# Kernel tuning notes

Measured on AMD Instinct MI355X. Metric: run time of the kernel, lower is better.

Reference implementation:

```python
import jax, jax.numpy as jnp
import numpy as np

D_MODEL = 256
D_INNER = 512   # expand=2 * d_model
D_STATE = 16
D_CONV = 4
DT_RANK = 16    # ceil(d_model/16)
N_BLOCKS = 5
BATCH = 8192
INPUT_DIM = 2048
NUM_CLASSES = 8


def setup_inputs() -> dict:
    key = jax.random.key(0)
    ks = jax.random.split(key, 10)
    rn = lambda k, shape, s: jax.random.normal(k, shape, jnp.float32) * s
    inp = {}
    inp['x'] = rn(ks[0], (BATCH, INPUT_DIM), 1.0)
    # preprocess Linear(input_dim, 256)
    inp['W_pre'] = rn(ks[1], (D_MODEL, INPUT_DIM), 0.02)
    inp['b_pre'] = jnp.zeros((D_MODEL,), jnp.float32)
    # per-block Mamba params, stacked over N_BLOCKS
    inp['in_proj_w'] = rn(ks[2], (N_BLOCKS, 2 * D_INNER, D_MODEL), 0.02)
    inp['conv_w'] = rn(ks[3], (N_BLOCKS, D_INNER, 1, D_CONV), 0.1)   # depthwise, groups=d_inner
    inp['conv_b'] = jnp.zeros((N_BLOCKS, D_INNER), jnp.float32)
    inp['x_proj_w'] = rn(ks[4], (N_BLOCKS, DT_RANK + 2 * D_STATE, D_INNER), 0.02)
    inp['dt_proj_w'] = rn(ks[5], (N_BLOCKS, D_INNER, DT_RANK), 0.1)
    inp['dt_proj_b'] = rn(ks[6], (N_BLOCKS, D_INNER), 0.1)
    # S4D-real init: A = 1..d_state, A_log = log(A)
    A = jnp.tile(jnp.arange(1, D_STATE + 1, dtype=jnp.float32)[None, None, :], (N_BLOCKS, D_INNER, 1))
    inp['A_log'] = jnp.log(A)
    inp['D'] = jnp.ones((N_BLOCKS, D_INNER), jnp.float32)
    inp['out_proj_w'] = rn(ks[7], (N_BLOCKS, D_MODEL, D_INNER), 0.02)
    inp['ln_g'] = jnp.ones((D_MODEL,), jnp.float32)
    inp['ln_b'] = jnp.zeros((D_MODEL,), jnp.float32)
    inp['W_cls'] = rn(ks[8], (NUM_CLASSES, D_MODEL), 0.02)
    inp['b_cls'] = jnp.zeros((NUM_CLASSES,), jnp.float32)
    return inp


def _mamba(x, in_w, cw, cb, xw, dtw, dtb, Alog, Dp, ow):
    # x: (B, L, d_model)
    B, L, _ = x.shape
    xz = jnp.einsum('bld,ed->ble', x, in_w)            # (B, L, 2*d_inner)
    xi, z = jnp.split(xz, 2, axis=-1)
    # causal depthwise conv1d over the sequence axis
    xt = xi.transpose(0, 2, 1)                         # (B, d_inner, L)
    xc = jax.lax.conv_general_dilated(
        xt, cw, window_strides=(1,), padding=[(D_CONV - 1, 0)],
        dimension_numbers=('NCH', 'OIH', 'NCH'), feature_group_count=D_INNER)
    xi = jax.nn.silu((xc + cb[None, :, None]).transpose(0, 2, 1))   # (B, L, d_inner)
    xdbl = jnp.einsum('bld,ed->ble', xi, xw)           # (B, L, dt_rank + 2*d_state)
    dt, Bm, Cm = jnp.split(xdbl, [DT_RANK, DT_RANK + D_STATE], axis=-1)
    dt = jax.nn.softplus(jnp.einsum('blr,dr->bld', dt, dtw) + dtb)  # (B, L, d_inner)
    A = -jnp.exp(Alog)                                  # (d_inner, d_state)
    dA = jnp.exp(dt[..., None] * A)                     # (B, L, d_inner, d_state)
    dBx = dt[..., None] * Bm[:, :, None, :] * xi[..., None]

    def step(h, t):
        dA_t, dBx_t, C_t = t
        h = dA_t * h + dBx_t                            # (B, d_inner, d_state)
        return h, jnp.einsum('bds,bs->bd', h, C_t)

    h0 = jnp.zeros((B, D_INNER, D_STATE), x.dtype)
    _, ys = jax.lax.scan(step, h0, (dA.swapaxes(0, 1), dBx.swapaxes(0, 1), Cm.swapaxes(0, 1)))
    y = ys.swapaxes(0, 1) + xi * Dp                     # (B, L, d_inner)
    y = y * jax.nn.silu(z)
    return jnp.einsum('bld,ed->ble', y, ow)             # (B, L, d_model)


def reference(x, W_pre, b_pre, in_proj_w, conv_w, conv_b, x_proj_w, dt_proj_w,
              dt_proj_b, A_log, D, out_proj_w, ln_g, ln_b, W_cls, b_cls):
    # dropout is identity in eval mode
    h = (x @ W_pre.T + b_pre)[:, None, :]               # (B, 1, 256)
    for i in range(N_BLOCKS):
        h = h + _mamba(h, in_proj_w[i], conv_w[i], conv_b[i], x_proj_w[i],
                       dt_proj_w[i], dt_proj_b[i], A_log[i], D[i], out_proj_w[i])
    mu = h.mean(-1, keepdims=True)
    var = ((h - mu) ** 2).mean(-1, keepdims=True)
    hn = (h - mu) * jax.lax.rsqrt(var + 1e-5) * ln_g + ln_b
    return hn[:, 0, :] @ W_cls.T + b_cls                # (B, num_classes)
```

## Files before the change

### kernel.cpp

```cpp
#include <hip/hip_runtime.h>
#include <hip/hip_bf16.h>

typedef __attribute__((ext_vector_type(8))) short bf16x8;
typedef __attribute__((ext_vector_type(4))) short s16x4;
typedef __attribute__((ext_vector_type(4))) float f32x4;
typedef __attribute__((ext_vector_type(4))) float float4v;

static __device__ __forceinline__ unsigned short f2b(float f) {
  unsigned int u = __builtin_bit_cast(unsigned int, f);
  u += 0x7fffu + ((u >> 16) & 1u);
  return (unsigned short)(u >> 16);
}
static __device__ __forceinline__ float b2f(unsigned short s) {
  unsigned int u = ((unsigned int)s) << 16;
  return __builtin_bit_cast(float, u);
}
static __device__ __forceinline__ float fsilu(float x) {
  float e = __builtin_amdgcn_exp2f(-1.44269504f * x);
  return x * __builtin_amdgcn_rcpf(1.f + e);
}
static __device__ __forceinline__ float fsoftplus(float a) {
  if (a > 20.f) return a;
  float t = __builtin_amdgcn_exp2f(1.44269504f * a);
  return 0.69314718f * __builtin_amdgcn_logf(1.f + t);
}
static __device__ __forceinline__ void gl16(const void* g, void* l) {
  __builtin_amdgcn_global_load_lds(
      (const __attribute__((address_space(1))) unsigned int*)g,
      (__attribute__((address_space(3))) unsigned int*)l, 16, 0, 0);
}
template <int N>
static __device__ __forceinline__ void waitv() {
  if constexpr (N == 0) asm volatile("s_waitcnt vmcnt(0)" ::: "memory");
  else if constexpr (N == 1) asm volatile("s_waitcnt vmcnt(1)" ::: "memory");
  else if constexpr (N == 2) asm volatile("s_waitcnt vmcnt(2)" ::: "memory");
  else if constexpr (N == 3) asm volatile("s_waitcnt vmcnt(3)" ::: "memory");
  else if constexpr (N == 4) asm volatile("s_waitcnt vmcnt(4)" ::: "memory");
  else if constexpr (N == 5) asm volatile("s_waitcnt vmcnt(5)" ::: "memory");
  else if constexpr (N == 6) asm volatile("s_waitcnt vmcnt(6)" ::: "memory");
  else if constexpr (N == 8) asm volatile("s_waitcnt vmcnt(8)" ::: "memory");
}
static __device__ __forceinline__ void lgkm_bar() {
  asm volatile("s_waitcnt lgkmcnt(0)" ::: "memory");
  __builtin_amdgcn_s_barrier();
}

template <int TM, int TN>
__global__ __launch_bounds__(256) void gemm_pl(
    const unsigned short* __restrict__ A, const unsigned short* __restrict__ W,
    int N, int K, int GY,
    const float* __restrict__ p0, float* __restrict__ of,
    unsigned short* __restrict__ ob) {
  constexpr int FM = TM / 32, FN = TN / 32;
  constexpr int IA = TM / 64, IW = TN / 64;
  constexpr int LPT = IA + IW;
  __shared__ __align__(16) unsigned short As[4][TM * 32];
  __shared__ __align__(16) unsigned short Ws[4][TN * 32];

  const int t = threadIdx.x, lane = t & 63, wave = t >> 6;
  const int lr = lane & 15;
  const int q = gridDim.x >> 3;
  const int s = (blockIdx.x & 7) * q + (blockIdx.x >> 3);
  const int bm = (s / GY) * TM, bn = (s % GY) * TN;
  const int wr = (wave >> 1) * (TM / 2), wc = (wave & 1) * (TN / 2);

  f32x4 acc[FM][FN];
#pragma unroll
  for (int i = 0; i < FM; ++i)
#pragma unroll
    for (int j = 0; j < FN; ++j) acc[i][j] = (f32x4){0.f, 0.f, 0.f, 0.f};

  const unsigned short* agB =
      A + (long)(bm + wave * (TM / 4) + (lane >> 2)) * K +
      ((lane & 3) ^ ((lane >> 3) & 3)) * 8;
  const unsigned short* wgB =
      W + (long)(bn + wave * (TN / 4) + (lane >> 2)) * K +
      ((lane & 3) ^ ((lane >> 3) & 3)) * 8;

  auto STAGE = [&](int k0, int b) {
#pragma unroll
    for (int j = 0; j < IA; ++j)
      gl16(agB + k0 + (long)j * 16 * K, &As[b][(wave * (TM / 4) + j * 16) * 32]);
#pragma unroll
    for (int j = 0; j < IW; ++j)
      gl16(wgB + k0 + (long)j * 16 * K, &Ws[b][(wave * (TN / 4) + j * 16) * 32]);
  };

  auto COMPUTE = [&](int b) {
    bf16x8 af[FM], bg[FN];
    const int sw = ((lane >> 4) ^ ((lane >> 1) & 3)) * 8;
#pragma unroll
    for (int m = 0; m < FM; ++m)
      af[m] = *(const bf16x8*)&As[b][(wr + m * 16 + lr) * 32 + sw];
#pragma unroll
    for (int n = 0; n < FN; ++n)
      bg[n] = *(const bf16x8*)&Ws[b][(wc + n * 16 + lr) * 32 + sw];
    __builtin_amdgcn_s_setprio(1);
#pragma unroll
    for (int m = 0; m < FM; ++m)
#pragma unroll
      for (int n = 0; n < FN; ++n)
        acc[m][n] = __builtin_amdgcn_mfma_f32_16x16x32_bf16(af[m], bg[n],
                                                            acc[m][n], 0, 0, 0);
    __builtin_amdgcn_s_setprio(0);
  };

  const int NT = K >> 5;
  STAGE(0, 0);
  STAGE(32, 1);
  for (int tt = 0; tt < NT; ++tt) {
    if (tt + 2 < NT) {
      STAGE((tt + 2) << 5, (tt + 2) & 3);
      waitv<2 * LPT>();
    } else if (tt + 1 < NT) {
      waitv<LPT>();
    } else {
      waitv<0>();
    }
    __builtin_amdgcn_s_barrier();
    COMPUTE(tt & 3);
    __builtin_amdgcn_sched_barrier(0);
  }

  const int m0 = bm + wr + (lane >> 4) * 4;
  const int n0 = bn + wc + lr;
#pragma unroll
  for (int mi = 0; mi < FM; ++mi)
#pragma unroll
    for (int ni = 0; ni < FN; ++ni) {
      const int n = n0 + ni * 16;
#pragma unroll
      for (int r = 0; r < 4; ++r) {
        const int m = m0 + mi * 16 + r;
        float v = acc[mi][ni][r] + p0[n];
        of[(long)m * N + n] = v;
        ob[(long)m * N + n] = f2b(v);
      }
    }
}

__global__ __launch_bounds__(512) void mamba5(
    const unsigned short* __restrict__ hb0, const float* __restrict__ h0,
    const unsigned short* __restrict__ inwb,
    const unsigned short* __restrict__ xwpb,
    const unsigned short* __restrict__ dtwpb,
    const unsigned short* __restrict__ owb,
    const float* __restrict__ conv_b, const float* __restrict__ dt_b,
    const float* __restrict__ Dp, float* __restrict__ hout) {
  __shared__ __align__(16) unsigned short SMEM[81216];
  unsigned short* XiL = SMEM;
  unsigned short* SzL = SMEM + 16384;
  unsigned short* Ring = SMEM + 32768;
  unsigned short* HLr = SMEM + 65536;
  float* Dxl = (float*)(SMEM + 73728);
  float* BCl = (float*)(SMEM + 78080);
  float* Par = (float*)(SMEM + 78144);

  const int t = threadIdx.x, lane = t & 63, w = t >> 6;
  const int lr = lane & 15, lg = lane >> 4;
  const int bm = blockIdx.x * 32;
  const int m04 = lg * 4;
  const int rg16 = (w >> 2) * 16;
  const int cg32 = (w & 3) * 32;
  const int strow = lane >> 2;
  const int stc = (lane & 3) ^ ((strow >> 1) & 3);

#pragma unroll
  for (int j = 0; j < 2; ++j) {
    const int i = w * 2 + j;
    const int row = 2 * i + (lane >> 5);
    const int c = (lane & 31) ^ (row & 7);
    gl16(hb0 + (long)(bm + row) * 256 + c * 8, HLr + i * 512);
  }
  float hres[2][2][4];
#pragma unroll
  for (int ng = 0; ng < 2; ++ng)
#pragma unroll
    for (int n = 0; n < 2; ++n)
#pragma unroll
      for (int r = 0; r < 4; ++r)
        hres[ng][n][r] = h0[(long)(bm + rg16 + m04 + r) * 256 + ng * 128 +
                            cg32 + n * 16 + lr];
  waitv<0>();
  __builtin_amdgcn_s_barrier();

  for (int blk = 0; blk < 5; ++blk) {
    const unsigned short* inw = inwb + (long)blk * 1024 * 256;
    const unsigned short* xwp = xwpb + (long)blk * 64 * 512;
    const unsigned short* dtwp = dtwpb + (long)blk * 512 * 32;
    const unsigned short* ow = owb + (long)blk * 256 * 512;
    const float* cbv = conv_b + blk * 512;
    const float* dtbv = dt_b + blk * 512;
    const float* Dv = Dp + blk * 512;

    auto STAGE1 = [&](int tt, int slot) {
      const int nt = tt >> 3, kq = tt & 7;
      gl16(inw + (long)(nt * 128 + w * 16 + strow) * 256 + kq * 32 + stc * 8,
           Ring + slot * 4096 + w * 512);
    };
    if (w < 6) {
      const float* ps = (w < 2) ? cbv + (w & 1) * 256
                      : (w < 4) ? dtbv + (w & 1) * 256
                                : Dv + (w & 1) * 256;
      gl16(ps + lane * 4, (unsigned short*)Par + w * 512);
    }
    STAGE1(0, 0); STAGE1(1, 1); STAGE1(2, 2); STAGE1(3, 3);
    STAGE1(4, 4); STAGE1(5, 5); STAGE1(6, 6);
    f32x4 acc1[2];
#pragma unroll
    for (int tt = 0; tt < 64; ++tt) {
      if (tt <= 57) waitv<6>();
      else if (tt == 58) waitv<5>();
      else if (tt == 59) waitv<4>();
      else if (tt == 60) waitv<3>();
      else if (tt == 61) waitv<2>();
      else if (tt == 62) waitv<1>();
      else waitv<0>();
      __builtin_amdgcn_s_barrier();
      if (tt + 7 < 64) STAGE1(tt + 7, (tt + 7) & 7);
      __builtin_amdgcn_sched_barrier(0);
      const int nt = tt >> 3, kq = tt & 7;
      if (kq == 0) {
#pragma unroll
        for (int n = 0; n < 2; ++n) {
          const int c = nt * 128 + cg32 + n * 16 + lr;
          const float cb = (nt < 4) ? Par[c] : 0.f;
          acc1[n] = (f32x4){cb, cb, cb, cb};
        }
      }
      const unsigned short* Bs = Ring + (tt & 7) * 4096;
      const int ar = rg16 + lr;
      bf16x8 af = *(const bf16x8*)
          &HLr[ar * 256 + (((kq * 4 + lg) ^ (ar & 7)) * 8)];
      bf16x8 bg[2];
#pragma unroll
      for (int n = 0; n < 2; ++n) {
        const int rb = cg32 + n * 16 + lr;
        bg[n] = *(const bf16x8*)&Bs[rb * 32 + ((lg ^ ((rb >> 1) & 3)) * 8)];
      }
      __builtin_amdgcn_s_setprio(1);
#pragma unroll
      for (int n = 0; n < 2; ++n)
        acc1[n] = __builtin_amdgcn_mfma_f32_16x16x32_bf16(af, bg[n], acc1[n],
                                                          0, 0, 0);
      __builtin_amdgcn_s_setprio(0);
      if (kq == 7) {
#pragma unroll
        for (int n = 0; n < 2; ++n) {
          const int c = nt * 128 + cg32 + n * 16 + lr;
#pragma unroll
          for (int r = 0; r < 4; ++r) {
            const int row = rg16 + m04 + r;
            const float v = fsilu(acc1[n][r]);
            if (nt < 4)
              XiL[row * 512 + (((c >> 3) ^ (row & 7)) * 8) + (c & 7)] = f2b(v);
            else
              SzL[row * 512 + (c - 512)] = f2b(v);
          }
        }
      }
      __builtin_amdgcn_sched_barrier(0);
    }
    lgkm_bar();

#pragma unroll
    for (int j = 0; j < 8; ++j) {
      const int i = w * 8 + j;
      gl16(xwp + (long)i * 512 + (lane ^ (i & 7)) * 8, Ring + i * 512);
    }
    waitv<0>();
    __builtin_amdgcn_s_barrier();
    {
      const int fm2 = w & 1, fn2 = w >> 1;
      const int ar = fm2 * 16 + lr, rb = fn2 * 16 + lr;
      f32x4 a2 = {0.f, 0.f, 0.f, 0.f};
      __builtin_amdgcn_s_setprio(1);
#pragma unroll
      for (int kc = 0; kc < 16; ++kc) {
        bf16x8 af = *(const bf16x8*)
            &XiL[ar * 512 + (((kc * 4 + lg) ^ (lr & 7)) * 8)];
        bf16x8 bg = *(const bf16x8*)
            &Ring[rb * 512 + (((kc * 4 + lg) ^ (lr & 7)) * 8)];
        a2 = __builtin_amdgcn_mfma_f32_16x16x32_bf16(af, bg, a2, 0, 0, 0);
      }
      __builtin_amdgcn_s_setprio(0);
#pragma unroll
      for (int r = 0; r < 4; ++r)
        Dxl[(fm2 * 16 + m04 + r) * 68 + fn2 * 16 + lr] = a2[r];
    }
    lgkm_bar();

#pragma unroll
    for (int j = 0; j < 4; ++j) {
      const int u = w * 4 + j;
      const int row = u * 16 + (lane >> 2);
      const int c = (lane & 3) ^ (row & 3);
      gl16(dtwp + (long)row * 32 + c * 8, Ring + u * 512);
    }
    if (t < 32) {
      float bc = 0.f;
      const float* dx = &Dxl[t * 68];
#pragma unroll
      for (int s2 = 0; s2 < 16; ++s2) bc += dx[16 + s2] * dx[32 + s2];
      BCl[t] = bc;
    }
    bf16x8 afdt;
    {
      const float* dx = &Dxl[((w & 1) * 16 + lr) * 68 + lg * 8];
#pragma unroll
      for (int e = 0; e < 8; ++e) afdt[e] = (short)f2b(dx[e]);
    }
    waitv<0>();
    lgkm_bar();

    {
      const int fn4 = w >> 1, m04b = (w & 1) * 16 + m04;
#pragma unroll
      for (int tt = 0; tt < 8; ++tt) {
        const int d = tt * 64 + fn4 * 16 + lr;
        bf16x8 bg = *(const bf16x8*)&Ring[d * 32 + ((lg ^ (d & 3)) * 8)];
        f32x4 da = __builtin_amdgcn_mfma_f32_16x16x32_bf16(
            afdt, bg, (f32x4){0.f, 0.f, 0.f, 0.f}, 0, 0, 0);
        const float dbv = Par[512 + d], dvv = Par[1024 + d];
#pragma unroll
        for (int r = 0; r < 4; ++r) {
          const int row = m04b + r;
          const float dtv = fsoftplus(da[r] + dbv);
          const int xoff = row * 512 + (((d >> 3) ^ (row & 7)) * 8) + (d & 7);
          const float y = b2f(XiL[xoff]) * (dtv * BCl[row] + dvv) *
                          b2f(SzL[row * 512 + d]);
          XiL[xoff] = f2b(y);
        }
      }
    }
    lgkm_bar();

    auto STAGE5 = [&](int tt, int slot) {
      const int ng = tt >> 4, kq = tt & 15;
      gl16(ow + (long)(ng * 128 + w * 16 + strow) * 512 + kq * 32 + stc * 8,
           Ring + slot * 4096 + w * 512);
    };
    STAGE5(0, 0); STAGE5(1, 1); STAGE5(2, 2); STAGE5(3, 3);
    STAGE5(4, 4); STAGE5(5, 5); STAGE5(6, 6);
    f32x4 acc5[2];
#pragma unroll
    for (int tt = 0; tt < 32; ++tt) {
      if (tt <= 25) waitv<6>();
      else if (tt == 26) waitv<5>();
      else if (tt == 27) waitv<4>();
      else if (tt == 28) waitv<3>();
      else if (tt == 29) waitv<2>();
      else if (tt == 30) waitv<1>();
      else waitv<0>();
      __builtin_amdgcn_s_barrier();
      if (tt + 7 < 32) STAGE5(tt + 7, (tt + 7) & 7);
      __builtin_amdgcn_sched_barrier(0);
      const int ng = tt >> 4, kq = tt & 15;
      if (kq == 0) {
        acc5[0] = (f32x4){0.f, 0.f, 0.f, 0.f};
        acc5[1] = (f32x4){0.f, 0.f, 0.f, 0.f};
      }
      const unsigned short* Bs = Ring + (tt & 7) * 4096;
      const int ar = rg16 + lr;
      bf16x8 af = *(const bf16x8*)
          &XiL[ar * 512 + (((kq * 4 + lg) ^ (ar & 7)) * 8)];
      bf16x8 bg[2];
#pragma unroll
      for (int n = 0; n < 2; ++n) {
        const int rb = cg32 + n * 16 + lr;
        bg[n] = *(const bf16x8*)&Bs[rb * 32 + ((lg ^ ((rb >> 1) & 3)) * 8)];
      }
      __builtin_amdgcn_s_setprio(1);
#pragma unroll
      for (int n = 0; n < 2; ++n)
        acc5[n] = __builtin_amdgcn_mfma_f32_16x16x32_bf16(af, bg[n], acc5[n],
                                                          0, 0, 0);
      __builtin_amdgcn_s_setprio(0);
      if (kq == 15) {
#pragma unroll
        for (int n = 0; n < 2; ++n) {
          const int col = ng * 128 + cg32 + n * 16 + lr;
#pragma unroll
          for (int r = 0; r < 4; ++r) {
            const int row = rg16 + m04 + r;
            const float v = acc5[n][r] + hres[ng][n][r];
            hres[ng][n][r] = v;
            HLr[row * 256 + (((col >> 3) ^ (row & 7)) * 8) + (col & 7)] =
                f2b(v);
          }
        }
      }
      __builtin_amdgcn_sched_barrier(0);
    }
    lgkm_bar();
  }

#pragma unroll
  for (int ng = 0; ng < 2; ++ng)
#pragma unroll
    for (int n = 0; n < 2; ++n)
#pragma unroll
      for (int r = 0; r < 4; ++r)
        hout[(long)(bm + rg16 + m04 + r) * 256 + ng * 128 + cg32 + n * 16 +
             lr] = hres[ng][n][r];
}

__global__ __launch_bounds__(256) void castx(const float* __restrict__ s,
                                             unsigned short* __restrict__ d) {
  const int n4 = (8192 * 2048) / 4;
  for (int i = blockIdx.x * 256 + threadIdx.x; i < n4; i += gridDim.x * 256) {
    float4v v = ((const float4v*)s)[i];
    s16x4 o;
    o[0] = (short)f2b(v[0]); o[1] = (short)f2b(v[1]);
    o[2] = (short)f2b(v[2]); o[3] = (short)f2b(v[3]);
    ((s16x4*)d)[i] = o;
  }
}

__global__ __launch_bounds__(256) void precast(
    const float* __restrict__ wpre, const float* __restrict__ inw,
    const float* __restrict__ ow, const float* __restrict__ xw,
    const float* __restrict__ dtw, const float* __restrict__ cw,
    unsigned short* __restrict__ wpreb, unsigned short* __restrict__ inwb,
    unsigned short* __restrict__ owb, unsigned short* __restrict__ xwpb,
    unsigned short* __restrict__ dtwpb) {
  const int S0 = 524288;
  const int S1 = S0 + 1310720;
  const int S2 = S1 + 655360;
  const int S3 = S2 + 163840;
  const int S4 = S3 + 81920;
  int i4 = (blockIdx.x * 256 + threadIdx.x) * 4;
  if (i4 >= S4) return;
  float4v v = {0.f, 0.f, 0.f, 0.f};
  unsigned short* dst;
  if (i4 < S0) {
    v = *(const float4v*)(wpre + i4);
    dst = wpreb + i4;
  } else if (i4 < S1) {
    int o = i4 - S0;
    v = *(const float4v*)(inw + o);
    int b = o >> 18, row = (o >> 8) & 1023;
    if (row < 512) {
      float c3 = cw[(b * 512 + row) * 4 + 3];
      v[0] *= c3; v[1] *= c3; v[2] *= c3; v[3] *= c3;
    }
    dst = inwb + o;
  } else if (i4 < S2) {
    int o = i4 - S1;
    v = *(const float4v*)(ow + o);
    dst = owb + o;
  } else if (i4 < S3) {
    int o = i4 - S2;
    dst = xwpb + o;
    int k = o & 511, j = (o >> 9) & 63, b = o >> 15;
    if (j < 48) v = *(const float4v*)(xw + ((long)(b * 48 + j)) * 512 + k);
  } else {
    int o = i4 - S3;
    dst = dtwpb + o;
    int k = o & 31, dd = o >> 5;
    if (k < 16) v = *(const float4v*)(dtw + (long)dd * 16 + k);
  }
  s16x4 sv;
  sv[0] = (short)f2b(v[0]); sv[1] = (short)f2b(v[1]);
  sv[2] = (short)f2b(v[2]); sv[3] = (short)f2b(v[3]);
  *(s16x4*)dst = sv;
}

__global__ __launch_bounds__(256) void final_ln_cls(
    const float* __restrict__ h, const float* __restrict__ g,
    const float* __restrict__ be, const float* __restrict__ Wc,
    const float* __restrict__ bc, float* __restrict__ out) {
  const int wave = threadIdx.x >> 6, lane = threadIdx.x & 63;
  const int row = blockIdx.x * 4 + wave;
  const float4v* hr = (const float4v*)(h + (long)row * 256);
  float4v v = hr[lane];
  float s = v[0] + v[1] + v[2] + v[3];
#pragma unroll
  for (int o = 32; o; o >>= 1) s += __shfl_xor(s, o);
  const float mu = s * (1.f / 256.f);
  float d0 = v[0] - mu, d1 = v[1] - mu, d2 = v[2] - mu, d3 = v[3] - mu;
  float qq = d0 * d0 + d1 * d1 + d2 * d2 + d3 * d3;
#pragma unroll
  for (int o = 32; o; o >>= 1) qq += __shfl_xor(qq, o);
  const float rs = rsqrtf(qq * (1.f / 256.f) + 1e-5f);
  const float4v gv = ((const float4v*)g)[lane];
  const float4v bv = ((const float4v*)be)[lane];
  float hn[4];
  hn[0] = d0 * rs * gv[0] + bv[0];
  hn[1] = d1 * rs * gv[1] + bv[1];
  hn[2] = d2 * rs * gv[2] + bv[2];
  hn[3] = d3 * rs * gv[3] + bv[3];
  float lg[8];
#pragma unroll
  for (int o = 0; o < 8; ++o) {
    const float4v wv = ((const float4v*)(Wc + o * 256))[lane];
    float p = hn[0] * wv[0] + hn[1] * wv[1] + hn[2] * wv[2] + hn[3] * wv[3];
#pragma unroll
    for (int x = 32; x; x >>= 1) p += __shfl_xor(p, x);
    lg[o] = p;
  }
  if (lane == 0) {
#pragma unroll
    for (int o = 0; o < 8; ++o) out[(long)row * 8 + o] = lg[o] + bc[o];
  }
}

extern "C" void kernel_launch(void* const* d_in, const int* in_sizes, int n_in,
                              void* d_out, int out_size, void* d_ws,
                              size_t ws_size, hipStream_t stream) {
  const float* x      = (const float*)d_in[0];
  const float* W_pre  = (const float*)d_in[1];
  const float* b_pre  = (const float*)d_in[2];
  const float* in_w   = (const float*)d_in[3];
  const float* conv_w = (const float*)d_in[4];
  const float* conv_b = (const float*)d_in[5];
  const float* x_w    = (const float*)d_in[6];
  const float* dt_w   = (const float*)d_in[7];
  const float* dt_b   = (const float*)d_in[8];
  const float* Dp     = (const float*)d_in[10];
  const float* out_w  = (const float*)d_in[11];
  const float* ln_g   = (const float*)d_in[12];
  const float* ln_b   = (const float*)d_in[13];
  const float* W_cls  = (const float*)d_in[14];
  const float* b_cls  = (const float*)d_in[15];
  float* out = (float*)d_out;

  char* w = (char*)d_ws;
  unsigned short* wpreb = (unsigned short*)w; w += 256 * 2048 * 2;
  unsigned short* inwb  = (unsigned short*)w; w += 5 * 1024 * 256 * 2;
  unsigned short* xwpb  = (unsigned short*)w; w += 5 * 64 * 512 * 2;
  unsigned short* owb   = (unsigned short*)w; w += 5 * 256 * 512 * 2;
  unsigned short* dtwpb = (unsigned short*)w; w += 5 * 512 * 32 * 2;
  float*          h     = (float*)w;          w += 8192 * 256 * 4;
  unsigned short* hb    = (unsigned short*)w; w += 8192 * 256 * 2;
  unsigned short* xb    = (unsigned short*)w; w += 8192 * 2048 * 2;

  precast<<<2672, 256, 0, stream>>>(W_pre, in_w, out_w, x_w, dt_w, conv_w,
                                    wpreb, inwb, owb, xwpb, dtwpb);
  castx<<<2048, 256, 0, stream>>>(x, xb);

  gemm_pl<128, 64><<<256, 256, 0, stream>>>(
      xb, wpreb, 256, 2048, 4, b_pre, h, hb);

  mamba5<<<256, 512, 0, stream>>>(hb, h, inwb, xwpb, dtwpb, owb,
                                  conv_b, dt_b, Dp, h);

  final_ln_cls<<<2048, 256, 0, stream>>>(h, ln_g, ln_b, W_cls, b_cls, out);
}
```

Measured before the change: 189.7 us.

## Double mamba5 block to 1024 threads with wider N tiles and shallower ring

The fused five-block Mamba kernel now runs 16 waves per workgroup instead of 8. Each wave covers a 32-column slice of a 256-wide N tile, which halves the number of in_proj and out_proj pipeline iterations. The weight ring drops from 8 slots of 4096 to 4 slots of 8192 with prefetch depth 3, and per-wave residual registers halve. The goal is more latency hiding and MFMA parallelism per CU, since only 256 workgroups exist. The cost is a shallower prefetch depth, idle waves in the x_proj stage, and the need for the dt/scan stage indexing to match the new wave count.

```diff
diff --git a/kernel.cpp b/kernel.cpp
--- a/kernel.cpp
+++ b/kernel.cpp
@@ -36,7 +36,6 @@
   else if constexpr (N == 2) asm volatile("s_waitcnt vmcnt(2)" ::: "memory");
   else if constexpr (N == 3) asm volatile("s_waitcnt vmcnt(3)" ::: "memory");
   else if constexpr (N == 4) asm volatile("s_waitcnt vmcnt(4)" ::: "memory");
-  else if constexpr (N == 5) asm volatile("s_waitcnt vmcnt(5)" ::: "memory");
   else if constexpr (N == 6) asm volatile("s_waitcnt vmcnt(6)" ::: "memory");
   else if constexpr (N == 8) asm volatile("s_waitcnt vmcnt(8)" ::: "memory");
 }
@@ -139,7 +138,7 @@
     }
 }
 
-__global__ __launch_bounds__(512) void mamba5(
+__global__ __launch_bounds__(1024) void mamba5(
     const unsigned short* __restrict__ hb0, const float* __restrict__ h0,
     const unsigned short* __restrict__ inwb,
     const unsigned short* __restrict__ xwpb,
@@ -160,27 +159,23 @@
   const int lr = lane & 15, lg = lane >> 4;
   const int bm = blockIdx.x * 32;
   const int m04 = lg * 4;
-  const int rg16 = (w >> 2) * 16;
-  const int cg32 = (w & 3) * 32;
+  const int rg16 = (w >> 3) * 16;
+  const int cg32 = (w & 7) * 32;
   const int strow = lane >> 2;
   const int stc = (lane & 3) ^ ((strow >> 1) & 3);
 
-#pragma unroll
-  for (int j = 0; j < 2; ++j) {
-    const int i = w * 2 + j;
-    const int row = 2 * i + (lane >> 5);
+  {
+    const int row = 2 * w + (lane >> 5);
     const int c = (lane & 31) ^ (row & 7);
-    gl16(hb0 + (long)(bm + row) * 256 + c * 8, HLr + i * 512);
-  }
-  float hres[2][2][4];
-#pragma unroll
-  for (int ng = 0; ng < 2; ++ng)
-#pragma unroll
-    for (int n = 0; n < 2; ++n)
-#pragma unroll
-      for (int r = 0; r < 4; ++r)
-        hres[ng][n][r] = h0[(long)(bm + rg16 + m04 + r) * 256 + ng * 128 +
-                            cg32 + n * 16 + lr];
+    gl16(hb0 + (long)(bm + row) * 256 + c * 8, HLr + w * 512);
+  }
+  float hres[2][4];
+#pragma unroll
+  for (int n = 0; n < 2; ++n)
+#pragma unroll
+    for (int r = 0; r < 4; ++r)
+      hres[n][r] =
+          h0[(long)(bm + rg16 + m04 + r) * 256 + cg32 + n * 16 + lr];
   waitv<0>();
   __builtin_amdgcn_s_barrier();
 
@@ -195,8 +190,8 @@
 
     auto STAGE1 = [&](int tt, int slot) {
       const int nt = tt >> 3, kq = tt & 7;
-      gl16(inw + (long)(nt * 128 + w * 16 + strow) * 256 + kq * 32 + stc * 8,
-           Ring + slot * 4096 + w * 512);
+      gl16(inw + (long)(nt * 256 + w * 16 + strow) * 256 + kq * 32 + stc * 8,
+           Ring + slot * 8192 + w * 512);
     };
     if (w < 6) {
       const float* ps = (w < 2) ? cbv + (w & 1) * 256
@@ -204,31 +199,26 @@
                                 : Dv + (w & 1) * 256;
       gl16(ps + lane * 4, (unsigned short*)Par + w * 512);
     }
-    STAGE1(0, 0); STAGE1(1, 1); STAGE1(2, 2); STAGE1(3, 3);
-    STAGE1(4, 4); STAGE1(5, 5); STAGE1(6, 6);
+    STAGE1(0, 0); STAGE1(1, 1); STAGE1(2, 2);
     f32x4 acc1[2];
 #pragma unroll
-    for (int tt = 0; tt < 64; ++tt) {
-      if (tt <= 57) waitv<6>();
-      else if (tt == 58) waitv<5>();
-      else if (tt == 59) waitv<4>();
-      else if (tt == 60) waitv<3>();
-      else if (tt == 61) waitv<2>();
-      else if (tt == 62) waitv<1>();
+    for (int tt = 0; tt < 32; ++tt) {
+      if (tt <= 29) waitv<2>();
+      else if (tt == 30) waitv<1>();
       else waitv<0>();
       __builtin_amdgcn_s_barrier();
-      if (tt + 7 < 64) STAGE1(tt + 7, (tt + 7) & 7);
+      if (tt + 3 < 32) STAGE1(tt + 3, (tt + 3) & 3);
       __builtin_amdgcn_sched_barrier(0);
       const int nt = tt >> 3, kq = tt & 7;
       if (kq == 0) {
 #pragma unroll
         for (int n = 0; n < 2; ++n) {
-          const int c = nt * 128 + cg32 + n * 16 + lr;
-          const float cb = (nt < 4) ? Par[c] : 0.f;
+          const int c = nt * 256 + cg32 + n * 16 + lr;
+          const float cb = (nt < 2) ? Par[c] : 0.f;
           acc1[n] = (f32x4){cb, cb, cb, cb};
         }
       }
-      const unsigned short* Bs = Ring + (tt & 7) * 4096;
+      const unsigned short* Bs = Ring + (tt & 3) * 8192;
       const int ar = rg16 + lr;
       bf16x8 af = *(const bf16x8*)
           &HLr[ar * 256 + (((kq * 4 + lg) ^ (ar & 7)) * 8)];
@@ -247,12 +237,12 @@
       if (kq == 7) {
 #pragma unroll
         for (int n = 0; n < 2; ++n) {
-          const int c = nt * 128 + cg32 + n * 16 + lr;
+          const int c = nt * 256 + cg32 + n * 16 + lr;
 #pragma unroll
           for (int r = 0; r < 4; ++r) {
             const int row = rg16 + m04 + r;
             const float v = fsilu(acc1[n][r]);
-            if (nt < 4)
+            if (nt < 2)
               XiL[row * 512 + (((c >> 3) ^ (row & 7)) * 8) + (c & 7)] = f2b(v);
             else
               SzL[row * 512 + (c - 512)] = f2b(v);
@@ -264,13 +254,13 @@
     lgkm_bar();
 
 #pragma unroll
-    for (int j = 0; j < 8; ++j) {
-      const int i = w * 8 + j;
+    for (int j = 0; j < 4; ++j) {
+      const int i = w * 4 + j;
       gl16(xwp + (long)i * 512 + (lane ^ (i & 7)) * 8, Ring + i * 512);
     }
     waitv<0>();
     __builtin_amdgcn_s_barrier();
-    {
+    if (w < 8) {
       const int fm2 = w & 1, fn2 = w >> 1;
       const int ar = fm2 * 16 + lr, rb = fn2 * 16 + lr;
       f32x4 a2 = {0.f, 0.f, 0.f, 0.f};
@@ -291,8 +281,8 @@
     lgkm_bar();
 
 #pragma unroll
-    for (int j = 0; j < 4; ++j) {
-      const int u = w * 4 + j;
+    for (int j = 0; j < 2; ++j) {
+      const int u = w * 2 + j;
       const int row = u * 16 + (lane >> 2);
       const int c = (lane & 3) ^ (row & 3);
       gl16(dtwp + (long)row * 32 + c * 8, Ring + u * 512);
@@ -314,10 +304,11 @@
     lgkm_bar();
 
     {
-      const int fn4 = w >> 1, m04b = (w & 1) * 16 + m04;
-#pragma unroll
-      for (int tt = 0; tt < 8; ++tt) {
-        const int d = tt * 64 + fn4 * 16 + lr;
+      const int fn4 = w >> 1;
+      const int m04b = (w & 1) * 16 + m04;
+#pragma unroll
+      for (int tt = 0; tt < 4; ++tt) {
+        const int d = tt * 128 + fn4 * 16 + lr;
         bf16x8 bg = *(const bf16x8*)&Ring[d * 32 + ((lg ^ (d & 3)) * 8)];
         f32x4 da = __builtin_amdgcn_mfma_f32_16x16x32_bf16(
             afdt, bg, (f32x4){0.f, 0.f, 0.f, 0.f}, 0, 0, 0);
@@ -336,34 +327,25 @@
     lgkm_bar();
 
     auto STAGE5 = [&](int tt, int slot) {
-      const int ng = tt >> 4, kq = tt & 15;
-      gl16(ow + (long)(ng * 128 + w * 16 + strow) * 512 + kq * 32 + stc * 8,
-           Ring + slot * 4096 + w * 512);
+      gl16(ow + (long)(w * 16 + strow) * 512 + tt * 32 + stc * 8,
+           Ring + slot * 8192 + w * 512);
     };
-    STAGE5(0, 0); STAGE5(1, 1); STAGE5(2, 2); STAGE5(3, 3);
-    STAGE5(4, 4); STAGE5(5, 5); STAGE5(6, 6);
+    STAGE5(0, 0); STAGE5(1, 1); STAGE5(2, 2);
     f32x4 acc5[2];
-#pragma unroll
-    for (int tt = 0; tt < 32; ++tt) {
-      if (tt <= 25) waitv<6>();
-      else if (tt == 26) waitv<5>();
-      else if (tt == 27) waitv<4>();
-      else if (tt == 28) waitv<3>();
-      else if (tt == 29) waitv<2>();
-      else if (tt == 30) waitv<1>();
+    acc5[0] = (f32x4){0.f, 0.f, 0.f, 0.f};
+    acc5[1] = (f32x4){0.f, 0.f, 0.f, 0.f};
+#pragma unroll
+    for (int tt = 0; tt < 16; ++tt) {
+      if (tt <= 13) waitv<2>();
+      else if (tt == 14) waitv<1>();
       else waitv<0>();
       __builtin_amdgcn_s_barrier();
-      if (tt + 7 < 32) STAGE5(tt + 7, (tt + 7) & 7);
+      if (tt + 3 < 16) STAGE5(tt + 3, (tt + 3) & 3);
       __builtin_amdgcn_sched_barrier(0);
-      const int ng = tt >> 4, kq = tt & 15;
-      if (kq == 0) {
-        acc5[0] = (f32x4){0.f, 0.f, 0.f, 0.f};
-        acc5[1] = (f32x4){0.f, 0.f, 0.f, 0.f};
-      }
-      const unsigned short* Bs = Ring + (tt & 7) * 4096;
+      const unsigned short* Bs = Ring + (tt & 3) * 8192;
       const int ar = rg16 + lr;
       bf16x8 af = *(const bf16x8*)
-          &XiL[ar * 512 + (((kq * 4 + lg) ^ (ar & 7)) * 8)];
+          &XiL[ar * 512 + (((tt * 4 + lg) ^ (ar & 7)) * 8)];
       bf16x8 bg[2];
 #pragma unroll
       for (int n = 0; n < 2; ++n) {
@@ -376,15 +358,15 @@
         acc5[n] = __builtin_amdgcn_mfma_f32_16x16x32_bf16(af, bg[n], acc5[n],
                                                           0, 0, 0);
       __builtin_amdgcn_s_setprio(0);
-      if (kq == 15) {
+      if (tt == 15) {
 #pragma unroll
         for (int n = 0; n < 2; ++n) {
-          const int col = ng * 128 + cg32 + n * 16 + lr;
+          const int col = cg32 + n * 16 + lr;
 #pragma unroll
           for (int r = 0; r < 4; ++r) {
             const int row = rg16 + m04 + r;
-            const float v = acc5[n][r] + hres[ng][n][r];
-            hres[ng][n][r] = v;
+            const float v = acc5[n][r] + hres[n][r];
+            hres[n][r] = v;
             HLr[row * 256 + (((col >> 3) ^ (row & 7)) * 8) + (col & 7)] =
                 f2b(v);
           }
@@ -396,13 +378,11 @@
   }
 
 #pragma unroll
-  for (int ng = 0; ng < 2; ++ng)
-#pragma unroll
-    for (int n = 0; n < 2; ++n)
-#pragma unroll
-      for (int r = 0; r < 4; ++r)
-        hout[(long)(bm + rg16 + m04 + r) * 256 + ng * 128 + cg32 + n * 16 +
-             lr] = hres[ng][n][r];
+  for (int n = 0; n < 2; ++n)
+#pragma unroll
+    for (int r = 0; r < 4; ++r)
+      hout[(long)(bm + rg16 + m04 + r) * 256 + cg32 + n * 16 + lr] =
+          hres[n][r];
 }
 
 __global__ __launch_bounds__(256) void castx(const float* __restrict__ s,
@@ -542,8 +522,8 @@
   gemm_pl<128, 64><<<256, 256, 0, stream>>>(
       xb, wpreb, 256, 2048, 4, b_pre, h, hb);
 
-  mamba5<<<256, 512, 0, stream>>>(hb, h, inwb, xwpb, dtwpb, owb,
-                                  conv_b, dt_b, Dp, h);
+  mamba5<<<256, 1024, 0, stream>>>(hb, h, inwb, xwpb, dtwpb, owb,
+                                   conv_b, dt_b, Dp, h);
 
   final_ln_cls<<<2048, 256, 0, stream>>>(h, ln_g, ln_b, W_cls, b_cls, out);
 }
```

Measured after the change: 231.7 us. +22.2%, slower.
